# Optimization experiments

Measured on AMD Instinct MI355X. Metric: run time of the kernel, lower is better.

## Reference

```python
import jax, jax.numpy as jnp
import numpy as np

N = 10           # node count hardcoded in original module
FEAT_IN = 3      # position(2) + orientation(1)
FEAT_OUT = 16    # 'simple' mode
FEAT_CC = 2 * FEAT_OUT
B = 16384
NEG_SLOPE = 0.2


def _pair_index():
    # Faithful pair ordering: for node i, row 0 is the self-pair (i,i),
    # rows 1..N-1 are j != i in ascending order.
    idx = np.empty((N, N), dtype=np.int32)
    for i in range(N):
        idx[i, 0] = i
        idx[i, 1:] = [j for j in range(N) if j != i]
    return jnp.asarray(idx)


def setup_inputs() -> dict:
    key = jax.random.key(0)
    ks = jax.random.split(key, 12)
    s = 0.1
    return {
        "position": jax.random.normal(ks[0], (B, N, 2), dtype=jnp.float32),
        "orientation": jax.random.normal(ks[1], (B, N, 1), dtype=jnp.float32),
        # preliminary_transform: Linear(3 -> 16)
        "Wp": jax.random.normal(ks[2], (FEAT_IN, FEAT_OUT), dtype=jnp.float32) * s,
        "bp": jax.random.normal(ks[3], (FEAT_OUT,), dtype=jnp.float32) * s,
        # connectivity_net: Linear(32->32), LReLU, Linear(32->8), LReLU, Linear(8->2)
        "W1": jax.random.normal(ks[4], (FEAT_CC, 32), dtype=jnp.float32) * s,
        "b1": jax.random.normal(ks[5], (32,), dtype=jnp.float32) * s,
        "W2": jax.random.normal(ks[6], (32, 8), dtype=jnp.float32) * s,
        "b2": jax.random.normal(ks[7], (8,), dtype=jnp.float32) * s,
        "W3": jax.random.normal(ks[8], (8, 2), dtype=jnp.float32) * s,
        "b3": jax.random.normal(ks[9], (2,), dtype=jnp.float32) * s,
    }


def reference(position, orientation, Wp, bp, W1, b1, W2, b2, W3, b3):
    lrelu = lambda x: jnp.where(x >= 0, x, NEG_SLOPE * x)
    # [B, N, 3] -> [B, N, 16]
    feat = jnp.concatenate([position, orientation], axis=2) @ Wp + bp
    idx = _pair_index()                                   # [N, N]
    vj = feat[:, idx]                                     # [B, N, N, 16] gathered partners
    vi = jnp.broadcast_to(feat[:, :, None, :], vj.shape)  # [B, N, N, 16] source node
    pair = jnp.concatenate([vi, vj], axis=-1)             # [B, N, N, 32]
    h = lrelu(pair @ W1 + b1)
    h = lrelu(h @ W2 + b2)
    big_edge = h @ W3 + b3                                # [B, N, N, 2]
    adjacency = jnp.argmax(big_edge, axis=3)              # [B, N, N]
    return big_edge, adjacency
```

## Files before the change

### kernel.cpp

```cpp
#include <hip/hip_runtime.h>


typedef float v2f __attribute__((ext_vector_type(2)));
typedef float v4f __attribute__((ext_vector_type(4)));

constexpr int G = 12;
constexpr int GB_STRIDE = 36;
constexpr float NEG = 0.2f;

__global__ __launch_bounds__(256, 4) void gpn_kernel(
    const float* __restrict__ pos,
    const float* __restrict__ ori,
    const float* __restrict__ Wp,
    const float* __restrict__ bp,
    const float* __restrict__ W1,
    const float* __restrict__ b1,
    const float* __restrict__ W2,
    const float* __restrict__ b2,
    const float* __restrict__ W3,
    const float* __restrict__ b3,
    float* __restrict__ out,
    int B)
{
    __shared__ float sM[3 * 64];
    __shared__ float sc[64];
    __shared__ float sgb[G * 10 * GB_STRIDE];

    const int t = threadIdx.x;
    const int bBase = blockIdx.x * G;
    const int remG = B - bBase;
    const int nLanes = ((remG < G) ? remG : G) * 10 * 2;

    if (t < 192) {
        const int d = t >> 6, k = t & 63;
        const int kk = k & 31;
        const int fo = (k < 32) ? 0 : 16;
        float acc = 0.f;
#pragma unroll
        for (int f = 0; f < 16; ++f)
            acc = fmaf(Wp[d * 16 + f], W1[(fo + f) * 32 + kk], acc);
        sM[d * 64 + k] = acc;
    } else {
        const int k = t - 192;
        const int kk = k & 31;
        const int fo = (k < 32) ? 0 : 16;
        float acc = 0.f;
#pragma unroll
        for (int f = 0; f < 16; ++f)
            acc = fmaf(bp[f], W1[(fo + f) * 32 + kk], acc);
        if (k < 32) acc += b1[k];
        sc[k] = acc;
    }
    __syncthreads();

    v4f ga[8];
    const int r = t >> 1;
    const int half = t & 1;
    const int g = r / 10;
    const int i = r - g * 10;
    if (t < nLanes) {
        const int node = bBase * 10 + r;
        const v2f p = ((const v2f*)pos)[node];
        const float o = ori[node];
        const v4f* m4 = (const v4f*)sM;
        const v4f* c4 = (const v4f*)sc;
        v4f* dst = (v4f*)&sgb[r * GB_STRIDE];
#pragma unroll
        for (int q = 0; q < 8; ++q) {
            v4f gg = c4[q];
            gg += p.x * m4[q];
            gg += p.y * m4[16 + q];
            gg += o   * m4[32 + q];
            ga[q] = gg;
        }
#pragma unroll
        for (int qq = 0; qq < 4; ++qq) {
            const int q = 8 + half * 4 + qq;
            v4f gg = c4[q];
            gg += p.x * m4[q];
            gg += p.y * m4[16 + q];
            gg += o   * m4[32 + q];
            dst[q - 8] = gg;
        }
    }
    __syncthreads();

    if (t < nLanes) {
        const v2f* w2p = (const v2f*)W2;
        const v2f* w3p = (const v2f*)W3;
        const v2f bb2_0 = ((const v2f*)b2)[0];
        const v2f bb2_1 = ((const v2f*)b2)[1];
        const v2f bb2_2 = ((const v2f*)b2)[2];
        const v2f bb2_3 = ((const v2f*)b2)[3];
        const v2f bb3   = ((const v2f*)b3)[0];

        const int eRow = (bBase + g) * 100 + i * 10;
        const size_t adjOff = (size_t)B * 200;

#pragma unroll
        for (int cc = 0; cc < 5; ++cc) {
            const int c = half * 5 + cc;
            const int j = (c == 0) ? i : (((c - 1) < i) ? (c - 1) : c);
            const v4f* src = (const v4f*)&sgb[(g * 10 + j) * GB_STRIDE];

            v2f a0 = bb2_0, a1 = bb2_1, a2 = bb2_2, a3 = bb2_3;
#pragma unroll
            for (int q = 0; q < 8; ++q) {
                const v4f s = ga[q] + src[q];
                const v4f h = __builtin_elementwise_max(s, s * NEG);
                const int k0 = 4 * q;
                a0 += h.x * w2p[4 * (k0 + 0) + 0];
                a1 += h.x * w2p[4 * (k0 + 0) + 1];
                a2 += h.x * w2p[4 * (k0 + 0) + 2];
                a3 += h.x * w2p[4 * (k0 + 0) + 3];
                a0 += h.y * w2p[4 * (k0 + 1) + 0];
                a1 += h.y * w2p[4 * (k0 + 1) + 1];
                a2 += h.y * w2p[4 * (k0 + 1) + 2];
                a3 += h.y * w2p[4 * (k0 + 1) + 3];
                a0 += h.z * w2p[4 * (k0 + 2) + 0];
                a1 += h.z * w2p[4 * (k0 + 2) + 1];
                a2 += h.z * w2p[4 * (k0 + 2) + 2];
                a3 += h.z * w2p[4 * (k0 + 2) + 3];
                a0 += h.w * w2p[4 * (k0 + 3) + 0];
                a1 += h.w * w2p[4 * (k0 + 3) + 1];
                a2 += h.w * w2p[4 * (k0 + 3) + 2];
                a3 += h.w * w2p[4 * (k0 + 3) + 3];
            }

            const v2f h20 = __builtin_elementwise_max(a0, a0 * NEG);
            const v2f h21 = __builtin_elementwise_max(a1, a1 * NEG);
            const v2f h22 = __builtin_elementwise_max(a2, a2 * NEG);
            const v2f h23 = __builtin_elementwise_max(a3, a3 * NEG);

            v2f ev = bb3;
            ev += h20.x * w3p[0];
            ev += h20.y * w3p[1];
            ev += h21.x * w3p[2];
            ev += h21.y * w3p[3];
            ev += h22.x * w3p[4];
            ev += h22.y * w3p[5];
            ev += h23.x * w3p[6];
            ev += h23.y * w3p[7];

            const int E = eRow + c;
            ((v2f*)out)[E] = ev;
            out[adjOff + E] = (ev.y > ev.x) ? 1.0f : 0.0f;
        }
    }
}

extern "C" void kernel_launch(void* const* d_in, const int* in_sizes, int n_in,
                              void* d_out, int out_size, void* d_ws, size_t ws_size,
                              hipStream_t stream) {
    const float* pos = (const float*)d_in[0];
    const float* ori = (const float*)d_in[1];
    const float* Wp  = (const float*)d_in[2];
    const float* bp  = (const float*)d_in[3];
    const float* W1  = (const float*)d_in[4];
    const float* b1  = (const float*)d_in[5];
    const float* W2  = (const float*)d_in[6];
    const float* b2  = (const float*)d_in[7];
    const float* W3  = (const float*)d_in[8];
    const float* b3  = (const float*)d_in[9];
    float* out = (float*)d_out;

    const int B = in_sizes[0] / 20;
    const int nBlocks = (B + G - 1) / G;

    gpn_kernel<<<nBlocks, 256, 0, stream>>>(pos, ori, Wp, bp, W1, b1, W2, b2,
                                            W3, b3, out, B);
}
```

Before: 103.5 us.

## Precompute fused weights in a separate kernel and interchange pair loop for W2 reuse

The folded Wp·W1 matrix and bias are now computed once by a single-block prologue kernel into workspace, instead of being recomputed by every block and staged through shared memory behind a barrier. The main kernel reads them from global memory. Its second-layer loop is also interchanged so each W2 weight set is loaded once and applied to all five partner pairs, with five sets of accumulators kept live. This cuts redundant per-block setup and scalar weight loads, at the cost of an extra kernel launch and higher register pressure under the 4-blocks-per-CU launch bound.

```diff
diff --git a/kernel.cpp b/kernel.cpp
--- a/kernel.cpp
+++ b/kernel.cpp
@@ -8,29 +8,12 @@
 constexpr int GB_STRIDE = 36;
 constexpr float NEG = 0.2f;
 
-__global__ __launch_bounds__(256, 4) void gpn_kernel(
-    const float* __restrict__ pos,
-    const float* __restrict__ ori,
-    const float* __restrict__ Wp,
-    const float* __restrict__ bp,
-    const float* __restrict__ W1,
-    const float* __restrict__ b1,
-    const float* __restrict__ W2,
-    const float* __restrict__ b2,
-    const float* __restrict__ W3,
-    const float* __restrict__ b3,
-    float* __restrict__ out,
-    int B)
+__global__ __launch_bounds__(256, 1) void fuse_kernel(
+    const float* __restrict__ Wp, const float* __restrict__ bp,
+    const float* __restrict__ W1, const float* __restrict__ b1,
+    float* __restrict__ ws)
 {
-    __shared__ float sM[3 * 64];
-    __shared__ float sc[64];
-    __shared__ float sgb[G * 10 * GB_STRIDE];
-
     const int t = threadIdx.x;
-    const int bBase = blockIdx.x * G;
-    const int remG = B - bBase;
-    const int nLanes = ((remG < G) ? remG : G) * 10 * 2;
-
     if (t < 192) {
         const int d = t >> 6, k = t & 63;
         const int kk = k & 31;
@@ -39,7 +22,7 @@
 #pragma unroll
         for (int f = 0; f < 16; ++f)
             acc = fmaf(Wp[d * 16 + f], W1[(fo + f) * 32 + kk], acc);
-        sM[d * 64 + k] = acc;
+        ws[d * 64 + k] = acc;
     } else {
         const int k = t - 192;
         const int kk = k & 31;
@@ -49,9 +32,30 @@
         for (int f = 0; f < 16; ++f)
             acc = fmaf(bp[f], W1[(fo + f) * 32 + kk], acc);
         if (k < 32) acc += b1[k];
-        sc[k] = acc;
+        ws[192 + k] = acc;
     }
-    __syncthreads();
+}
+
+__global__ __launch_bounds__(256, 4) void gpn_kernel(
+    const float* __restrict__ pos,
+    const float* __restrict__ ori,
+    const float* __restrict__ ws,
+    const float* __restrict__ W2,
+    const float* __restrict__ b2,
+    const float* __restrict__ W3,
+    const float* __restrict__ b3,
+    float* __restrict__ out,
+    int B)
+{
+    __shared__ float sgb[G * 10 * GB_STRIDE];
+
+    const int t = threadIdx.x;
+    const int bBase = blockIdx.x * G;
+    const int remG = B - bBase;
+    const int nLanes = ((remG < G) ? remG : G) * 10 * 2;
+
+    const v4f* m4 = (const v4f*)ws;
+    const v4f* c4 = (const v4f*)(ws + 192);
 
     v4f ga[8];
     const int r = t >> 1;
@@ -62,8 +66,6 @@
         const int node = bBase * 10 + r;
         const v2f p = ((const v2f*)pos)[node];
         const float o = ori[node];
-        const v4f* m4 = (const v4f*)sM;
-        const v4f* c4 = (const v4f*)sc;
         v4f* dst = (v4f*)&sgb[r * GB_STRIDE];
 #pragma unroll
         for (int q = 0; q < 8; ++q) {
@@ -94,43 +96,55 @@
         const v2f bb2_3 = ((const v2f*)b2)[3];
         const v2f bb3   = ((const v2f*)b3)[0];
 
+        const v4f* src[5];
+#pragma unroll
+        for (int e = 0; e < 5; ++e) {
+            const int c = half * 5 + e;
+            const int j = (c == 0) ? i : (((c - 1) < i) ? (c - 1) : c);
+            src[e] = (const v4f*)&sgb[(g * 10 + j) * GB_STRIDE];
+        }
+
+        v2f A[5][4];
+#pragma unroll
+        for (int e = 0; e < 5; ++e) {
+            A[e][0] = bb2_0; A[e][1] = bb2_1; A[e][2] = bb2_2; A[e][3] = bb2_3;
+        }
+
+#pragma unroll
+        for (int q = 0; q < 8; ++q) {
+            const v4f gaq = ga[q];
+            const int k0 = 4 * q;
+            const v2f w00 = w2p[4 * (k0 + 0) + 0], w01 = w2p[4 * (k0 + 0) + 1],
+                      w02 = w2p[4 * (k0 + 0) + 2], w03 = w2p[4 * (k0 + 0) + 3];
+            const v2f w10 = w2p[4 * (k0 + 1) + 0], w11 = w2p[4 * (k0 + 1) + 1],
+                      w12 = w2p[4 * (k0 + 1) + 2], w13 = w2p[4 * (k0 + 1) + 3];
+            const v2f w20 = w2p[4 * (k0 + 2) + 0], w21 = w2p[4 * (k0 + 2) + 1],
+                      w22 = w2p[4 * (k0 + 2) + 2], w23 = w2p[4 * (k0 + 2) + 3];
+            const v2f w30 = w2p[4 * (k0 + 3) + 0], w31 = w2p[4 * (k0 + 3) + 1],
+                      w32 = w2p[4 * (k0 + 3) + 2], w33 = w2p[4 * (k0 + 3) + 3];
+#pragma unroll
+            for (int e = 0; e < 5; ++e) {
+                const v4f s = gaq + src[e][q];
+                const v4f h = __builtin_elementwise_max(s, s * NEG);
+                A[e][0] += h.x * w00; A[e][1] += h.x * w01;
+                A[e][2] += h.x * w02; A[e][3] += h.x * w03;
+                A[e][0] += h.y * w10; A[e][1] += h.y * w11;
+                A[e][2] += h.y * w12; A[e][3] += h.y * w13;
+                A[e][0] += h.z * w20; A[e][1] += h.z * w21;
+                A[e][2] += h.z * w22; A[e][3] += h.z * w23;
+                A[e][0] += h.w * w30; A[e][1] += h.w * w31;
+                A[e][2] += h.w * w32; A[e][3] += h.w * w33;
+            }
+        }
+
         const int eRow = (bBase + g) * 100 + i * 10;
         const size_t adjOff = (size_t)B * 200;
-
 #pragma unroll
-        for (int cc = 0; cc < 5; ++cc) {
-            const int c = half * 5 + cc;
-            const int j = (c == 0) ? i : (((c - 1) < i) ? (c - 1) : c);
-            const v4f* src = (const v4f*)&sgb[(g * 10 + j) * GB_STRIDE];
-
-            v2f a0 = bb2_0, a1 = bb2_1, a2 = bb2_2, a3 = bb2_3;
-#pragma unroll
-            for (int q = 0; q < 8; ++q) {
-                const v4f s = ga[q] + src[q];
-                const v4f h = __builtin_elementwise_max(s, s * NEG);
-                const int k0 = 4 * q;
-                a0 += h.x * w2p[4 * (k0 + 0) + 0];
-                a1 += h.x * w2p[4 * (k0 + 0) + 1];
-                a2 += h.x * w2p[4 * (k0 + 0) + 2];
-                a3 += h.x * w2p[4 * (k0 + 0) + 3];
-                a0 += h.y * w2p[4 * (k0 + 1) + 0];
-                a1 += h.y * w2p[4 * (k0 + 1) + 1];
-                a2 += h.y * w2p[4 * (k0 + 1) + 2];
-                a3 += h.y * w2p[4 * (k0 + 1) + 3];
-                a0 += h.z * w2p[4 * (k0 + 2) + 0];
-                a1 += h.z * w2p[4 * (k0 + 2) + 1];
-                a2 += h.z * w2p[4 * (k0 + 2) + 2];
-                a3 += h.z * w2p[4 * (k0 + 2) + 3];
-                a0 += h.w * w2p[4 * (k0 + 3) + 0];
-                a1 += h.w * w2p[4 * (k0 + 3) + 1];
-                a2 += h.w * w2p[4 * (k0 + 3) + 2];
-                a3 += h.w * w2p[4 * (k0 + 3) + 3];
-            }
-
-            const v2f h20 = __builtin_elementwise_max(a0, a0 * NEG);
-            const v2f h21 = __builtin_elementwise_max(a1, a1 * NEG);
-            const v2f h22 = __builtin_elementwise_max(a2, a2 * NEG);
-            const v2f h23 = __builtin_elementwise_max(a3, a3 * NEG);
+        for (int e = 0; e < 5; ++e) {
+            const v2f h20 = __builtin_elementwise_max(A[e][0], A[e][0] * NEG);
+            const v2f h21 = __builtin_elementwise_max(A[e][1], A[e][1] * NEG);
+            const v2f h22 = __builtin_elementwise_max(A[e][2], A[e][2] * NEG);
+            const v2f h23 = __builtin_elementwise_max(A[e][3], A[e][3] * NEG);
 
             v2f ev = bb3;
             ev += h20.x * w3p[0];
@@ -142,7 +156,7 @@
             ev += h23.x * w3p[6];
             ev += h23.y * w3p[7];
 
-            const int E = eRow + c;
+            const int E = eRow + half * 5 + e;
             ((v2f*)out)[E] = ev;
             out[adjOff + E] = (ev.y > ev.x) ? 1.0f : 0.0f;
         }
@@ -163,10 +177,11 @@
     const float* W3  = (const float*)d_in[8];
     const float* b3  = (const float*)d_in[9];
     float* out = (float*)d_out;
+    float* ws  = (float*)d_ws;
 
     const int B = in_sizes[0] / 20;
     const int nBlocks = (B + G - 1) / G;
 
-    gpn_kernel<<<nBlocks, 256, 0, stream>>>(pos, ori, Wp, bp, W1, b1, W2, b2,
-                                            W3, b3, out, B);
+    fuse_kernel<<<1, 256, 0, stream>>>(Wp, bp, W1, b1, ws);
+    gpn_kernel<<<nBlocks, 256, 0, stream>>>(pos, ori, ws, W2, b2, W3, b3, out, B);
 }
```

Result: faster. 95.17 us (-8.1%).
